# Performance work log

Measured on AMD Instinct MI355X. Metric: run time of the kernel, lower is better.

The kernel has to match this reference:

```python
import jax, jax.numpy as jnp
import numpy as np

IN_F, OUT_F, LAT, B = 1024, 1024, 16, 256


def setup_inputs() -> dict:
    key = jax.random.key(0)
    ks = jax.random.split(key, 6)
    # xavier_normal for weight [in, out]
    std_w = float(np.sqrt(2.0 / (IN_F + OUT_F)))
    weight = jax.random.normal(ks[0], (IN_F, OUT_F), dtype=jnp.float32) * std_w
    bias = jnp.full((OUT_F,), 0.01, dtype=jnp.float32)
    # nn.Linear(latent, in): weight [in, latent], bias [in], kaiming-uniform-ish init
    lim = float(1.0 / np.sqrt(LAT))
    lt_w = jax.random.uniform(ks[1], (IN_F, LAT), minval=-lim, maxval=lim, dtype=jnp.float32)
    lt_b = jax.random.uniform(ks[2], (IN_F,), minval=-lim, maxval=lim, dtype=jnp.float32)
    tensor = jax.random.normal(ks[3], (B, IN_F), dtype=jnp.float32)
    z = jax.random.normal(ks[4], (B, LAT), dtype=jnp.float32)
    return {"tensor": tensor, "z": z, "weight": weight, "bias": bias,
            "lt_w": lt_w, "lt_b": lt_b}


def reference(tensor, z, weight, bias, lt_w, lt_b):
    # s = latent_transform(z): [B, in]
    s = z @ lt_w.T + lt_b
    # Demodulation factor: rsqrt(sum_i (s_i * W_io)^2 + eps) = rsqrt((s^2) @ (W^2) + eps)
    # Algebraically identical to forming the per-sample modulated weight, but
    # never materializes the [B, in, out] tensor.
    factor = jax.lax.rsqrt((s * s) @ (weight * weight) + 1e-8)  # [B, out]
    # x @ (W * s[:, :, None]) == (x * s) @ W
    out = ((tensor * s) @ weight) * factor + bias  # [B, out]
    return out
```

## Files before the change

kernel.cpp:

```cpp
#include <hip/hip_runtime.h>
#include <hip/hip_bf16.h>

constexpr int IN_F  = 1024;
constexpr int OUT_F = 1024;
constexpr int LAT   = 16;
constexpr int BATCH = 256;

typedef __attribute__((ext_vector_type(8))) short  bf16x8;
typedef __attribute__((ext_vector_type(4))) float  f32x4;

static __device__ __forceinline__ unsigned short bf16_bits(float v) {
  __hip_bfloat16 h = __float2bfloat16(v);
  return *reinterpret_cast<unsigned short*>(&h);
}
static __device__ __forceinline__ float bf16_f32(unsigned short u) {
  __hip_bfloat16 h;
  *reinterpret_cast<unsigned short*>(&h) = u;
  return __bfloat162float(h);
}

__global__ __launch_bounds__(256) void fused_mod(
    const float* __restrict__ tensor, const float* __restrict__ z,
    const float* __restrict__ lt_w, const float* __restrict__ lt_b,
    const float* __restrict__ W, const float* __restrict__ bias,
    float* __restrict__ out) {
  __shared__ __hip_bfloat16 s_lds[32 * 1024];
  __shared__ __hip_bfloat16 wbuf[4][2][2][32 * 64];

  const int bid = blockIdx.x;
  const int t = threadIdx.x;
  const int n0 = (bid & 31) * 32;
  const int m0 = (bid >> 5) * 32;
  const int lane = t & 63;
  const int wave = t >> 6;
  const int lm = lane & 15;
  const int h = lane >> 4;

  {
    const int koct = h & 1;
    bf16x8 zfrag[2];
#pragma unroll
    for (int bh = 0; bh < 2; ++bh) {
      const float* zp = z + (m0 + bh * 16 + lm) * LAT + koct * 8;
      float4 v0 = *reinterpret_cast<const float4*>(zp);
      float4 v1 = *reinterpret_cast<const float4*>(zp + 4);
      float v[8] = {v0.x, v0.y, v0.z, v0.w, v1.x, v1.y, v1.z, v1.w};
      union { unsigned short u[8]; bf16x8 b; } fz;
#pragma unroll
      for (int j = 0; j < 8; ++j) {
        unsigned short hi = bf16_bits(v[j]);
        fz.u[j] = (h < 2) ? hi : bf16_bits(v[j] - bf16_f32(hi));
      }
      zfrag[bh] = fz.b;
    }
#pragma unroll 4
    for (int itl = 0; itl < 16; ++itl) {
      const int i0 = (wave * 16 + itl) * 16;
      const float* wp = lt_w + (i0 + lm) * LAT + koct * 8;
      float4 v0 = *reinterpret_cast<const float4*>(wp);
      float4 v1 = *reinterpret_cast<const float4*>(wp + 4);
      float v[8] = {v0.x, v0.y, v0.z, v0.w, v1.x, v1.y, v1.z, v1.w};
      union { unsigned short u[8]; bf16x8 b; } f1, f2;
#pragma unroll
      for (int j = 0; j < 8; ++j) {
        unsigned short hi = bf16_bits(v[j]);
        f1.u[j] = hi;
        f2.u[j] = (h < 2) ? bf16_bits(v[j] - bf16_f32(hi)) : 0;
      }
      const float4 bq = *reinterpret_cast<const float4*>(lt_b + i0 + h * 4);
      const int cbase = (i0 >> 3) + (h >> 1);
      const int sub8 = (h & 1) * 8;
#pragma unroll
      for (int bh = 0; bh < 2; ++bh) {
        f32x4 sacc = {0.f, 0.f, 0.f, 0.f};
        sacc = __builtin_amdgcn_mfma_f32_16x16x32_bf16(f1.b, zfrag[bh], sacc, 0, 0, 0);
        sacc = __builtin_amdgcn_mfma_f32_16x16x32_bf16(f2.b, zfrag[bh], sacc, 0, 0, 0);
        const int r = bh * 16 + lm;
        union { unsigned short u[4]; uint2 d; } pk;
        pk.u[0] = bf16_bits(sacc[0] + bq.x);
        pk.u[1] = bf16_bits(sacc[1] + bq.y);
        pk.u[2] = bf16_bits(sacc[2] + bq.z);
        pk.u[3] = bf16_bits(sacc[3] + bq.w);
        const int off = r * 2048 + ((cbase ^ (r & 7)) << 4) + sub8;
        *reinterpret_cast<uint2*>(reinterpret_cast<char*>(s_lds) + off) = pk.d;
      }
    }
  }
  __syncthreads();

  const int sn  = lane & 31;
  const int shb = lane >> 5;

  f32x4 acc1[2][2], acc2[2][2];
#pragma unroll
  for (int mi = 0; mi < 2; ++mi)
#pragma unroll
    for (int ni = 0; ni < 2; ++ni) {
      acc1[mi][ni] = (f32x4){0.f, 0.f, 0.f, 0.f};
      acc2[mi][ni] = (f32x4){0.f, 0.f, 0.f, 0.f};
    }

#pragma unroll
  for (int tt = 0; tt < 4; ++tt) {
    const int k0 = (wave * 4 + tt) * 64;
    char* wt = reinterpret_cast<char*>(&wbuf[wave][tt & 1][0][0]);
    char* w2 = reinterpret_cast<char*>(&wbuf[wave][tt & 1][1][0]);
#pragma unroll
    for (int q = 0; q < 4; ++q) {
      const int koct = shb + 2 * q;
      union { unsigned short u[8]; bf16x8 b; } pw, pw2;
#pragma unroll
      for (int j = 0; j < 8; ++j) {
        const float v = W[(k0 + koct * 8 + j) * OUT_F + n0 + sn];
        pw.u[j]  = bf16_bits(v);
        pw2.u[j] = bf16_bits(v * v);
      }
      const int woff = sn * 128 + ((koct ^ (sn & 7)) << 4);
      *reinterpret_cast<bf16x8*>(wt + woff) = pw.b;
      *reinterpret_cast<bf16x8*>(w2 + woff) = pw2.b;
    }
#pragma unroll
    for (int sub = 0; sub < 2; ++sub) {
      const int kk = k0 + sub * 32 + h * 8;
      const int c = kk >> 3;
      union { unsigned short u[8]; bf16x8 b; } fxs0, fss0, fxs1, fss1;
      {
        const int r0 = lm;
        const float* xp0 = tensor + (m0 + r0) * IN_F + kk;
        float4 xa0 = *reinterpret_cast<const float4*>(xp0);
        float4 xb0 = *reinterpret_cast<const float4*>(xp0 + 4);
        bf16x8 s80 = *reinterpret_cast<const bf16x8*>(
            reinterpret_cast<char*>(s_lds) + r0 * 2048 + ((c ^ (r0 & 7)) << 4));
        const float xv0[8] = {xa0.x, xa0.y, xa0.z, xa0.w, xb0.x, xb0.y, xb0.z, xb0.w};
#pragma unroll
        for (int j = 0; j < 8; ++j) {
          const float sf = bf16_f32((unsigned short)s80[j]);
          fxs0.u[j] = bf16_bits(xv0[j] * sf);
          fss0.u[j] = bf16_bits(sf * sf);
        }
        const int r1 = 16 + lm;
        const float* xp1 = tensor + (m0 + r1) * IN_F + kk;
        float4 xa1 = *reinterpret_cast<const float4*>(xp1);
        float4 xb1 = *reinterpret_cast<const float4*>(xp1 + 4);
        bf16x8 s81 = *reinterpret_cast<const bf16x8*>(
            reinterpret_cast<char*>(s_lds) + r1 * 2048 + ((c ^ (r1 & 7)) << 4));
        const float xv1[8] = {xa1.x, xa1.y, xa1.z, xa1.w, xb1.x, xb1.y, xb1.z, xb1.w};
#pragma unroll
        for (int j = 0; j < 8; ++j) {
          const float sf = bf16_f32((unsigned short)s81[j]);
          fxs1.u[j] = bf16_bits(xv1[j] * sf);
          fss1.u[j] = bf16_bits(sf * sf);
        }
      }
#pragma unroll
      for (int ni = 0; ni < 2; ++ni) {
        const int br = ni * 16 + lm;
        const int boff = br * 128 + (((sub * 4 + h) ^ (br & 7)) << 4);
        bf16x8 b1 = *reinterpret_cast<const bf16x8*>(wt + boff);
        bf16x8 b2 = *reinterpret_cast<const bf16x8*>(w2 + boff);
        acc1[0][ni] = __builtin_amdgcn_mfma_f32_16x16x32_bf16(fxs0.b, b1, acc1[0][ni], 0, 0, 0);
        acc2[0][ni] = __builtin_amdgcn_mfma_f32_16x16x32_bf16(fss0.b, b2, acc2[0][ni], 0, 0, 0);
        acc1[1][ni] = __builtin_amdgcn_mfma_f32_16x16x32_bf16(fxs1.b, b1, acc1[1][ni], 0, 0, 0);
        acc2[1][ni] = __builtin_amdgcn_mfma_f32_16x16x32_bf16(fss1.b, b2, acc2[1][ni], 0, 0, 0);
      }
    }
  }

  {
    float* cb = reinterpret_cast<float*>(&wbuf[wave][0][0][0]);
#pragma unroll
    for (int mi = 0; mi < 2; ++mi)
#pragma unroll
      for (int ni = 0; ni < 2; ++ni) {
        const int i1 = mi * 2 + ni;
        *reinterpret_cast<f32x4*>(cb + i1 * 256 + lane * 4) = acc1[mi][ni];
        *reinterpret_cast<f32x4*>(cb + (4 + i1) * 256 + lane * 4) = acc2[mi][ni];
      }
  }
  __syncthreads();

  {
    const int mi = wave >> 1;
    const int ni = wave & 1;
    const int i1 = mi * 2 + ni;
    f32x4 t1 = {0.f, 0.f, 0.f, 0.f};
    f32x4 t2 = {0.f, 0.f, 0.f, 0.f};
#pragma unroll
    for (int v = 0; v < 4; ++v) {
      const float* src = reinterpret_cast<const float*>(&wbuf[v][0][0][0]);
      t1 += *reinterpret_cast<const f32x4*>(src + i1 * 256 + lane * 4);
      t2 += *reinterpret_cast<const f32x4*>(src + (4 + i1) * 256 + lane * 4);
    }
    const int col = n0 + ni * 16 + lm;
    const float bs = bias[col];
#pragma unroll
    for (int q = 0; q < 4; ++q) {
      const int row = m0 + mi * 16 + h * 4 + q;
      out[row * OUT_F + col] = t1[q] * __frsqrt_rn(t2[q] + 1e-8f) + bs;
    }
  }
}

extern "C" void kernel_launch(void* const* d_in, const int* in_sizes, int n_in,
                              void* d_out, int out_size, void* d_ws, size_t ws_size,
                              hipStream_t stream) {
  const float* tensor = (const float*)d_in[0];
  const float* z      = (const float*)d_in[1];
  const float* W      = (const float*)d_in[2];
  const float* bias   = (const float*)d_in[3];
  const float* lt_w   = (const float*)d_in[4];
  const float* lt_b   = (const float*)d_in[5];
  float* out = (float*)d_out;

  fused_mod<<<256, 256, 0, stream>>>(tensor, z, lt_w, lt_b, W, bias, out);
}
```

Measured before the change: 15.29 us.

## Split K across eight waves and square W fragments in registers

Doubles the block to 512 threads so eight waves each take a 128-wide K slice. This halves the serial per-wave K loop and the per-wave latent-transform work. The W-squared tile is no longer staged in LDS; each wave squares its bf16 W fragment in registers just before the MFMA, which frees LDS for the wider wave count. The cross-wave reduction now sums eight partials and needs an extra barrier plus a pass through s_lds. The costs are extra VALU work per MFMA, lower occupancy from the larger blocks, and a slight precision change, since W² is now the square of the already-rounded bf16 value.

```diff
diff --git a/kernel.cpp b/kernel.cpp
--- a/kernel.cpp
+++ b/kernel.cpp
@@ -19,13 +19,13 @@
   return __bfloat162float(h);
 }
 
-__global__ __launch_bounds__(256) void fused_mod(
+__global__ __launch_bounds__(512) void fused_mod(
     const float* __restrict__ tensor, const float* __restrict__ z,
     const float* __restrict__ lt_w, const float* __restrict__ lt_b,
     const float* __restrict__ W, const float* __restrict__ bias,
     float* __restrict__ out) {
-  __shared__ __hip_bfloat16 s_lds[32 * 1024];
-  __shared__ __hip_bfloat16 wbuf[4][2][2][32 * 64];
+  __shared__ __attribute__((aligned(16))) __hip_bfloat16 s_lds[32 * 1024];
+  __shared__ __attribute__((aligned(16))) __hip_bfloat16 wbuf[8][2][32 * 64];
 
   const int bid = blockIdx.x;
   const int t = threadIdx.x;
@@ -54,8 +54,8 @@
       zfrag[bh] = fz.b;
     }
 #pragma unroll 4
-    for (int itl = 0; itl < 16; ++itl) {
-      const int i0 = (wave * 16 + itl) * 16;
+    for (int itl = 0; itl < 8; ++itl) {
+      const int i0 = (wave * 8 + itl) * 16;
       const float* wp = lt_w + (i0 + lm) * LAT + koct * 8;
       float4 v0 = *reinterpret_cast<const float4*>(wp);
       float4 v1 = *reinterpret_cast<const float4*>(wp + 4);
@@ -101,23 +101,20 @@
     }
 
 #pragma unroll
-  for (int tt = 0; tt < 4; ++tt) {
-    const int k0 = (wave * 4 + tt) * 64;
-    char* wt = reinterpret_cast<char*>(&wbuf[wave][tt & 1][0][0]);
-    char* w2 = reinterpret_cast<char*>(&wbuf[wave][tt & 1][1][0]);
+  for (int tt = 0; tt < 2; ++tt) {
+    const int k0 = wave * 128 + tt * 64;
+    char* wt = reinterpret_cast<char*>(&wbuf[wave][tt & 1][0]);
 #pragma unroll
     for (int q = 0; q < 4; ++q) {
       const int koct = shb + 2 * q;
-      union { unsigned short u[8]; bf16x8 b; } pw, pw2;
+      union { unsigned short u[8]; bf16x8 b; } pw;
 #pragma unroll
       for (int j = 0; j < 8; ++j) {
         const float v = W[(k0 + koct * 8 + j) * OUT_F + n0 + sn];
-        pw.u[j]  = bf16_bits(v);
-        pw2.u[j] = bf16_bits(v * v);
+        pw.u[j] = bf16_bits(v);
       }
       const int woff = sn * 128 + ((koct ^ (sn & 7)) << 4);
       *reinterpret_cast<bf16x8*>(wt + woff) = pw.b;
-      *reinterpret_cast<bf16x8*>(w2 + woff) = pw2.b;
     }
 #pragma unroll
     for (int sub = 0; sub < 2; ++sub) {
@@ -157,17 +154,22 @@
         const int br = ni * 16 + lm;
         const int boff = br * 128 + (((sub * 4 + h) ^ (br & 7)) << 4);
         bf16x8 b1 = *reinterpret_cast<const bf16x8*>(wt + boff);
-        bf16x8 b2 = *reinterpret_cast<const bf16x8*>(w2 + boff);
-        acc1[0][ni] = __builtin_amdgcn_mfma_f32_16x16x32_bf16(fxs0.b, b1, acc1[0][ni], 0, 0, 0);
-        acc2[0][ni] = __builtin_amdgcn_mfma_f32_16x16x32_bf16(fss0.b, b2, acc2[0][ni], 0, 0, 0);
-        acc1[1][ni] = __builtin_amdgcn_mfma_f32_16x16x32_bf16(fxs1.b, b1, acc1[1][ni], 0, 0, 0);
-        acc2[1][ni] = __builtin_amdgcn_mfma_f32_16x16x32_bf16(fss1.b, b2, acc2[1][ni], 0, 0, 0);
+        union { unsigned short u[8]; bf16x8 b; } b2;
+#pragma unroll
+        for (int j = 0; j < 8; ++j) {
+          const float wv = bf16_f32((unsigned short)b1[j]);
+          b2.u[j] = bf16_bits(wv * wv);
+        }
+        acc1[0][ni] = __builtin_amdgcn_mfma_f32_16x16x32_bf16(fxs0.b, b1,   acc1[0][ni], 0, 0, 0);
+        acc2[0][ni] = __builtin_amdgcn_mfma_f32_16x16x32_bf16(fss0.b, b2.b, acc2[0][ni], 0, 0, 0);
+        acc1[1][ni] = __builtin_amdgcn_mfma_f32_16x16x32_bf16(fxs1.b, b1,   acc1[1][ni], 0, 0, 0);
+        acc2[1][ni] = __builtin_amdgcn_mfma_f32_16x16x32_bf16(fss1.b, b2.b, acc2[1][ni], 0, 0, 0);
       }
     }
   }
 
   {
-    float* cb = reinterpret_cast<float*>(&wbuf[wave][0][0][0]);
+    float* cb = reinterpret_cast<float*>(&wbuf[wave][0][0]);
 #pragma unroll
     for (int mi = 0; mi < 2; ++mi)
 #pragma unroll
@@ -180,23 +182,29 @@
   __syncthreads();
 
   {
-    const int mi = wave >> 1;
-    const int ni = wave & 1;
-    const int i1 = mi * 2 + ni;
-    f32x4 t1 = {0.f, 0.f, 0.f, 0.f};
-    f32x4 t2 = {0.f, 0.f, 0.f, 0.f};
-#pragma unroll
-    for (int v = 0; v < 4; ++v) {
-      const float* src = reinterpret_cast<const float*>(&wbuf[v][0][0][0]);
-      t1 += *reinterpret_cast<const f32x4*>(src + i1 * 256 + lane * 4);
-      t2 += *reinterpret_cast<const f32x4*>(src + (4 + i1) * 256 + lane * 4);
-    }
-    const int col = n0 + ni * 16 + lm;
-    const float bs = bias[col];
-#pragma unroll
-    for (int q = 0; q < 4; ++q) {
-      const int row = m0 + mi * 16 + h * 4 + q;
-      out[row * OUT_F + col] = t1[q] * __frsqrt_rn(t2[q] + 1e-8f) + bs;
+    f32x4 tsum = {0.f, 0.f, 0.f, 0.f};
+#pragma unroll
+    for (int v = 0; v < 8; ++v) {
+      const float* src = reinterpret_cast<const float*>(&wbuf[v][0][0]);
+      tsum += *reinterpret_cast<const f32x4*>(src + wave * 256 + lane * 4);
+    }
+    if (wave >= 4) {
+      *reinterpret_cast<f32x4*>(
+          reinterpret_cast<float*>(s_lds) + (wave - 4) * 256 + lane * 4) = tsum;
+    }
+    __syncthreads();
+    if (wave < 4) {
+      f32x4 t2 = *reinterpret_cast<const f32x4*>(
+          reinterpret_cast<const float*>(s_lds) + wave * 256 + lane * 4);
+      const int mi = wave >> 1;
+      const int ni = wave & 1;
+      const int col = n0 + ni * 16 + lm;
+      const float bs = bias[col];
+#pragma unroll
+      for (int q = 0; q < 4; ++q) {
+        const int row = m0 + mi * 16 + h * 4 + q;
+        out[row * OUT_F + col] = tsum[q] * __frsqrt_rn(t2[q] + 1e-8f) + bs;
+      }
     }
   }
 }
@@ -212,5 +220,5 @@
   const float* lt_b   = (const float*)d_in[5];
   float* out = (float*)d_out;
 
-  fused_mod<<<256, 256, 0, stream>>>(tensor, z, lt_w, lt_b, W, bias, out);
-}
+  fused_mod<<<256, 512, 0, stream>>>(tensor, z, lt_w, lt_b, W, bias, out);
+}
```

Measured after the change: 14.76 us. 3.4% less time.
